# Optimization experiments

Hardware: AMD Instinct MI355X
Metric: run time of the kernel (lower is better)

The kernel has to match this reference:

```python
import jax, jax.numpy as jnp
import numpy as np

B, H, W, C = 16, 64, 64, 192
NH, WS, SHIFT = 6, 8, 4          # heads, window size, shift (window//2)
DEPTH, MLP_R = 2, 4
N = WS * WS                      # tokens per window = 64
HD = C // NH                     # head dim = 32
SCALE = HD ** -0.5
TBL = (2 * WS - 1) ** 2          # relative-bias table size = 225
NW = (H // WS) * (W // WS)       # windows per image = 64


def _rel_pos_index():
    coords = np.stack(np.meshgrid(np.arange(WS), np.arange(WS), indexing='ij')).reshape(2, -1)
    rel = (coords[:, :, None] - coords[:, None, :]).transpose(1, 2, 0)
    rel[..., 0] += WS - 1
    rel[..., 1] += WS - 1
    rel[..., 0] *= 2 * WS - 1
    return jnp.asarray(rel.sum(-1))  # [N, N] int


def _attn_mask():
    # Swin shifted-window mask: region ids then pairwise -100 where ids differ.
    img = np.zeros((H, W))
    sl = (slice(0, -WS), slice(-WS, -SHIFT), slice(-SHIFT, None))
    cnt = 0
    for hs in sl:
        for ws in sl:
            img[hs, ws] = cnt
            cnt += 1
    mw = img.reshape(H // WS, WS, W // WS, WS).transpose(0, 2, 1, 3).reshape(-1, N)
    diff = mw[:, None, :] - mw[:, :, None]
    return jnp.asarray(np.where(diff != 0, -100.0, 0.0).astype(np.float32))  # [NW, N, N]


REL_IDX = _rel_pos_index()
ATTN_MASK = _attn_mask()


def _ln(x, g, b, eps=1e-5):
    mu = x.mean(-1, keepdims=True)
    var = ((x - mu) ** 2).mean(-1, keepdims=True)
    return (x - mu) * jax.lax.rsqrt(var + eps) * g + b


def setup_inputs() -> dict:
    key = jax.random.key(0)
    ks = jax.random.split(key, 8)
    s = 0.02
    return {
        'x': jax.random.normal(ks[0], (B, H * W, C), jnp.float32),
        'norm1_g': jnp.ones((DEPTH, C)), 'norm1_b': jnp.zeros((DEPTH, C)),
        'qkv_w': jax.random.normal(ks[1], (DEPTH, 3 * C, C)) * s,
        'qkv_b': jnp.zeros((DEPTH, 3 * C)),
        'bias_table': jax.random.normal(ks[2], (DEPTH, TBL, NH)) * s,
        'proj_w': jax.random.normal(ks[3], (DEPTH, C, C)) * s,
        'proj_b': jnp.zeros((DEPTH, C)),
        'norm2_g': jnp.ones((DEPTH, C)), 'norm2_b': jnp.zeros((DEPTH, C)),
        'fc1_w': jax.random.normal(ks[4], (DEPTH, MLP_R * C, C)) * s,
        'fc1_b': jnp.zeros((DEPTH, MLP_R * C)),
        'fc2_w': jax.random.normal(ks[5], (DEPTH, C, MLP_R * C)) * s,
        'fc2_b': jnp.zeros((DEPTH, C)),
    }


def _block(x, shift, n1g, n1b, qw, qb, tbl, pw, pb, n2g, n2b, f1w, f1b, f2w, f2b):
    shortcut = x
    y = _ln(x, n1g, n1b).reshape(B, H, W, C)
    if shift > 0:
        y = jnp.roll(y, (-shift, -shift), axis=(1, 2))
    # window partition -> [B*NW, N, C]
    win = y.reshape(B, H // WS, WS, W // WS, WS, C).transpose(0, 1, 3, 2, 4, 5).reshape(-1, N, C)
    qkv = (win @ qw.T + qb).reshape(-1, N, 3, NH, HD).transpose(2, 0, 3, 1, 4)
    q, k, v = qkv[0] * SCALE, qkv[1], qkv[2]          # each [B*NW, NH, N, HD]
    attn = jnp.einsum('bhnd,bhmd->bhnm', q, k)
    attn = attn + tbl[REL_IDX].transpose(2, 0, 1)[None]  # relative position bias
    if shift > 0:
        attn = (attn.reshape(B, NW, NH, N, N) + ATTN_MASK[None, :, None]).reshape(-1, NH, N, N)
    attn = jax.nn.softmax(attn, axis=-1)
    o = jnp.einsum('bhnm,bhmd->bhnd', attn, v).transpose(0, 2, 1, 3).reshape(-1, N, C)
    o = o @ pw.T + pb
    # window reverse
    y = o.reshape(B, H // WS, W // WS, WS, WS, C).transpose(0, 1, 3, 2, 4, 5).reshape(B, H, W, C)
    if shift > 0:
        y = jnp.roll(y, (shift, shift), axis=(1, 2))
    x = shortcut + y.reshape(B, H * W, C)
    h = _ln(x, n2g, n2b)
    h = jax.nn.gelu(h @ f1w.T + f1b, approximate=False)  # torch nn.GELU = exact erf
    return x + (h @ f2w.T + f2b)


def reference(x, norm1_g, norm1_b, qkv_w, qkv_b, bias_table, proj_w, proj_b,
              norm2_g, norm2_b, fc1_w, fc1_b, fc2_w, fc2_b):
    for i in range(DEPTH):
        shift = 0 if i % 2 == 0 else SHIFT
        x = _block(x, shift, norm1_g[i], norm1_b[i], qkv_w[i], qkv_b[i], bias_table[i],
                   proj_w[i], proj_b[i], norm2_g[i], norm2_b[i],
                   fc1_w[i], fc1_b[i], fc2_w[i], fc2_b[i])
    return x
```

## Files before the change

kernel.cpp:

```cpp
#include <hip/hip_runtime.h>
#include <hip/hip_bf16.h>
#include <math.h>

typedef __hip_bfloat16 bf16;
typedef short bf16x8 __attribute__((ext_vector_type(8)));
typedef short s16x4 __attribute__((ext_vector_type(4)));
typedef float f32x4 __attribute__((ext_vector_type(4)));

#define TOKENS 65536
#define C_ 192

__device__ __forceinline__ float b2f(bf16 v){ return __bfloat162float(v); }
__device__ __forceinline__ bf16 f2b(float v){ return __float2bfloat16(v); }
__device__ __forceinline__ short f2s(float v){
  bf16 b = __float2bfloat16(v);
  union { bf16 b; short s; } u; u.b = b; return u.s;
}
__device__ __forceinline__ float s2f(short s){
  union { unsigned u; float f; } c; c.u = ((unsigned)(unsigned short)s) << 16; return c.f;
}

struct WPtrs { const void* p[13]; };
#define W_TOTAL_ 892480
#define NELEM_ (TOKENS*C_)
__global__ void convert_k(WPtrs wp, const void* __restrict__ x,
                          bf16* __restrict__ canon, float* __restrict__ xf){
  const int offs[13] = {0, 384, 768, 221952, 223104, 225856, 299584,
                        299968, 300352, 300736, 595648, 597184, 892096};
  const int lens[13] = {384, 384, 221184, 1152, 2700, 73728, 384,
                        384, 384, 294912, 1536, 294912, 384};
  int flag = (*(const unsigned*)wp.p[0] == 0x3F800000u) ? 1 : 0;
  int i = blockIdx.x*blockDim.x + threadIdx.x;
  if (i < W_TOTAL_){
    int t = 0;
    while (t < 12 && i >= offs[t+1]) t++;
    int j = i - offs[t];
    if (j < lens[t]){
      if (flag) canon[i] = f2b(((const float*)wp.p[t])[j]);
      else      canon[i] = ((const bf16*)wp.p[t])[j];
    }
  } else {
    int j = i - W_TOTAL_;
    if (j < NELEM_){
      if (flag) xf[j] = ((const float*)x)[j];
      else      xf[j] = b2f(((const bf16*)x)[j]);
    }
  }
}
__global__ void outconv_k(const float* __restrict__ x, void* __restrict__ y, int n,
                          const unsigned* __restrict__ g){
  int flag = (g[0] == 0x3F800000u) ? 1 : 0;
  int i = blockIdx.x*blockDim.x + threadIdx.x;
  if (i >= n) return;
  if (flag) ((float*)y)[i] = x[i];
  else      ((bf16*)y)[i]  = f2b(x[i]);
}

__global__ void setup_k(const bf16* __restrict__ bt, float* __restrict__ biasF,
                        const bf16* __restrict__ f1w, const bf16* __restrict__ f2w,
                        bf16* __restrict__ w1p, bf16* __restrict__ w2p){
  int idx = blockIdx.x*blockDim.x + threadIdx.x;
  if (idx < 2*6*64*64){
    int v = idx & 63;
    int lane = (idx >> 6) & 63;
    int rest = idx >> 12;
    int head = rest % 6, dd = rest / 6;
    int jt = v >> 4, it = (v >> 2) & 3, r = v & 3;
    int quad = lane >> 4, lr = lane & 15;
    int j = jt*16 + quad*4 + r;
    int i = it*16 + lr;
    int rel = ((i>>3) - (j>>3) + 7)*15 + ((i&7) - (j&7) + 7);
    biasF[idx] = b2f(bt[(dd*225 + rel)*6 + head]);
    return;
  }
  int id = idx - 2*6*64*64;
  if (id >= 589824) return;
  int arr = id / 294912;
  int r = id % 294912;
  int d = r / 147456;
  int e = r % 147456;
  int j = e & 7, lane = (e >> 3) & 63, frag = e >> 9;
  int lr = lane & 15, quad = lane >> 4;
  if (arr == 0){
    int ks = frag % 6, t = frag / 6;
    int mh = t & 1, cc = t >> 1;
    w1p[(size_t)d*147456 + e] =
        f1w[(size_t)d*147456 + (size_t)(cc*32 + mh*16 + lr)*192 + ks*32 + quad*8 + j];
  } else {
    int ct = frag % 12, cc = frag / 12;
    w2p[(size_t)d*147456 + e] =
        f2w[(size_t)d*147456 + (size_t)(ct*16 + lr)*768 + cc*32 + quad*8 + j];
  }
}

__global__ __launch_bounds__(768, 1) void attn_fused_k(float* __restrict__ xres,
    const bf16* __restrict__ n1g, const bf16* __restrict__ n1b,
    const bf16* __restrict__ qw, const bf16* __restrict__ qb,
    const bf16* __restrict__ pw, const bf16* __restrict__ pb,
    const float* __restrict__ biasF, int shift)
{
  extern __shared__ char smem[];
  short* xo = (short*)smem;
  int win = blockIdx.x;
  int tid = threadIdx.x;
  int wave = tid >> 6, lane = tid & 63;
  int quad = lane >> 4, lr = lane & 15;
  int head = wave >> 1, half = wave & 1;
  int b_ = win >> 6, wl = win & 63, wh = wl >> 3, wwi = wl & 7;
  short* kh  = (short*)(smem + 25600 + head*18432);
  short* vth = kh + 2560;
  short* qP  = vth + 2304;

  int c0 = lane*3;
  float g0 = b2f(n1g[c0]), g1 = b2f(n1g[c0+1]), g2 = b2f(n1g[c0+2]);
  float e0 = b2f(n1b[c0]), e1 = b2f(n1b[c0+1]), e2 = b2f(n1b[c0+2]);
  #pragma unroll
  for (int p = 0; p < 6; p++){
    int tok = p*12 + wave;
    if (tok < 64){
      int hh = (wh*8 + (tok>>3) + shift) & 63, ww = (wwi*8 + (tok&7) + shift) & 63;
      const float* rowp = xres + ((size_t)(b_<<12) + (hh<<6) + ww)*C_;
      float v0 = rowp[c0], v1 = rowp[c0+1], v2 = rowp[c0+2];
      float s = v0+v1+v2;
      #pragma unroll
      for (int off=32; off; off>>=1) s += __shfl_xor(s, off);
      float mu = s * (1.0f/192.0f);
      float d0=v0-mu, d1=v1-mu, d2=v2-mu;
      float q = d0*d0+d1*d1+d2*d2;
      #pragma unroll
      for (int off=32; off; off>>=1) q += __shfl_xor(q, off);
      float rstd = rsqrtf(q*(1.0f/192.0f) + 1e-5f);
      xo[tok*200 + c0]   = f2s(d0*rstd*g0 + e0);
      xo[tok*200 + c0+1] = f2s(d1*rstd*g1 + e1);
      xo[tok*200 + c0+2] = f2s(d2*rstd*g2 + e2);
    }
  }
  __syncthreads();

  const short* qwd = (const short*)qw;
  #pragma unroll
  for (int cc = 0; cc < 3; cc++){
    int nbase = cc*192 + head*32;
    f32x4 acc[2][2];
    #pragma unroll
    for (int mt = 0; mt < 2; mt++)
      #pragma unroll
      for (int nt = 0; nt < 2; nt++) acc[mt][nt] = (f32x4){0.f,0.f,0.f,0.f};
    #pragma unroll
    for (int ks = 0; ks < 6; ks++){
      bf16x8 af[2], bx[2];
      #pragma unroll
      for (int mt = 0; mt < 2; mt++)
        af[mt] = *(const bf16x8*)(qwd + (size_t)(nbase + mt*16 + lr)*192 + ks*32 + quad*8);
      #pragma unroll
      for (int nt = 0; nt < 2; nt++)
        bx[nt] = *(const bf16x8*)&xo[((2*half + nt)*16 + lr)*200 + ks*32 + quad*8];
      #pragma unroll
      for (int mt = 0; mt < 2; mt++)
        #pragma unroll
        for (int nt = 0; nt < 2; nt++)
          acc[mt][nt] = __builtin_amdgcn_mfma_f32_16x16x32_bf16(af[mt], bx[nt], acc[mt][nt], 0, 0, 0);
    }
    #pragma unroll
    for (int mt = 0; mt < 2; mt++){
      float bv[4];
      #pragma unroll
      for (int r = 0; r < 4; r++) bv[r] = b2f(qb[nbase + mt*16 + quad*4 + r]);
      #pragma unroll
      for (int nt = 0; nt < 2; nt++){
        int tok = (2*half + nt)*16 + lr;
        if (cc == 0){
          s16x4 pk;
          #pragma unroll
          for (int r = 0; r < 4; r++) pk[r] = f2s((acc[mt][nt][r] + bv[r]) * 0.17677669529663689f);
          *(s16x4*)&qP[tok*40 + mt*16 + quad*4] = pk;
        } else if (cc == 1){
          s16x4 pk;
          #pragma unroll
          for (int r = 0; r < 4; r++) pk[r] = f2s(acc[mt][nt][r] + bv[r]);
          *(s16x4*)&kh[tok*40 + mt*16 + quad*4] = pk;
        } else {
          #pragma unroll
          for (int r = 0; r < 4; r++)
            vth[(mt*16 + quad*4 + r)*72 + tok] = f2s(acc[mt][nt][r] + bv[r]);
        }
      }
    }
  }
  __syncthreads();

  bf16x8 ak[4], bq[2];
  #pragma unroll
  for (int jt = 0; jt < 4; jt++) ak[jt] = *(const bf16x8*)&kh[(jt*16 + lr)*40 + quad*8];
  #pragma unroll
  for (int it = 0; it < 2; it++)
    bq[it] = *(const bf16x8*)&qP[((2*half + it)*16 + lr)*40 + quad*8];
  __syncthreads();

  f32x4 S[4][2];
  #pragma unroll
  for (int jt = 0; jt < 4; jt++)
    #pragma unroll
    for (int it = 0; it < 2; it++) S[jt][it] = (f32x4){0.f,0.f,0.f,0.f};
  #pragma unroll
  for (int jt = 0; jt < 4; jt++)
    #pragma unroll
    for (int it = 0; it < 2; it++)
      S[jt][it] = __builtin_amdgcn_mfma_f32_16x16x32_bf16(ak[jt], bq[it], S[jt][it], 0, 0, 0);

  const f32x4* bm = (const f32x4*)(biasF + ((size_t)head*64 + lane)*64);
  #pragma unroll
  for (int jt = 0; jt < 4; jt++)
    #pragma unroll
    for (int it = 0; it < 2; it++) S[jt][it] += bm[jt*4 + 2*half + it];

  if (shift){
    int idi[2];
    #pragma unroll
    for (int it = 0; it < 2; it++){
      int itg = 2*half + it;
      int hh = wh*8 + itg*2 + (lr >> 3);
      int wwc = wwi*8 + (lr & 7);
      idi[it] = (hh < 56 ? 0 : (hh < 60 ? 1 : 2))*3 + (wwc < 56 ? 0 : (wwc < 60 ? 1 : 2));
    }
    #pragma unroll
    for (int jt = 0; jt < 4; jt++)
      #pragma unroll
      for (int r = 0; r < 4; r++){
        int j = jt*16 + quad*4 + r;
        int hh = wh*8 + (j >> 3), wwc = wwi*8 + (j & 7);
        int idj = (hh < 56 ? 0 : (hh < 60 ? 1 : 2))*3 + (wwc < 56 ? 0 : (wwc < 60 ? 1 : 2));
        #pragma unroll
        for (int it = 0; it < 2; it++)
          if (idj != idi[it]) S[jt][it][r] -= 100.f;
      }
  }
  #pragma unroll
  for (int it = 0; it < 2; it++){
    float m = -1e30f;
    #pragma unroll
    for (int jt = 0; jt < 4; jt++)
      #pragma unroll
      for (int r = 0; r < 4; r++) m = fmaxf(m, S[jt][it][r]);
    m = fmaxf(m, __shfl_xor(m, 16));
    m = fmaxf(m, __shfl_xor(m, 32));
    float s = 0.f;
    #pragma unroll
    for (int jt = 0; jt < 4; jt++)
      #pragma unroll
      for (int r = 0; r < 4; r++){
        float e = __expf(S[jt][it][r] - m);
        S[jt][it][r] = e; s += e;
      }
    s += __shfl_xor(s, 16);
    s += __shfl_xor(s, 32);
    float inv = 1.0f / s;
    #pragma unroll
    for (int jt = 0; jt < 4; jt++){
      s16x4 pk;
      #pragma unroll
      for (int r = 0; r < 4; r++) pk[r] = f2s(S[jt][it][r] * inv);
      *(s16x4*)&qP[((2*half + it)*16 + lr)*68 + jt*16 + quad*4] = pk;
    }
  }
  __syncthreads();

  bf16x8 va[2][2], pv[2][2];
  #pragma unroll
  for (int mt = 0; mt < 2; mt++)
    #pragma unroll
    for (int ks = 0; ks < 2; ks++)
      va[mt][ks] = *(const bf16x8*)&vth[(mt*16 + lr)*72 + ks*32 + quad*8];
  #pragma unroll
  for (int nt = 0; nt < 2; nt++)
    #pragma unroll
    for (int ks = 0; ks < 2; ks++)
      pv[nt][ks] = *(const bf16x8*)&qP[((2*half + nt)*16 + lr)*68 + ks*32 + quad*8];

  f32x4 O[2][2];
  #pragma unroll
  for (int mt = 0; mt < 2; mt++)
    #pragma unroll
    for (int nt = 0; nt < 2; nt++) O[mt][nt] = (f32x4){0.f,0.f,0.f,0.f};
  #pragma unroll
  for (int mt = 0; mt < 2; mt++)
    #pragma unroll
    for (int nt = 0; nt < 2; nt++)
      #pragma unroll
      for (int ks = 0; ks < 2; ks++)
        O[mt][nt] = __builtin_amdgcn_mfma_f32_16x16x32_bf16(va[mt][ks], pv[nt][ks], O[mt][nt], 0, 0, 0);

  #pragma unroll
  for (int mt = 0; mt < 2; mt++)
    #pragma unroll
    for (int nt = 0; nt < 2; nt++){
      s16x4 pk;
      #pragma unroll
      for (int r = 0; r < 4; r++) pk[r] = f2s(O[mt][nt][r]);
      *(s16x4*)&xo[((2*half + nt)*16 + lr)*200 + head*32 + mt*16 + quad*4] = pk;
    }
  __syncthreads();

  int wm = wave / 6, wn = wave % 6;
  f32x4 po[2][2];
  #pragma unroll
  for (int mt = 0; mt < 2; mt++)
    #pragma unroll
    for (int nt = 0; nt < 2; nt++) po[mt][nt] = (f32x4){0.f,0.f,0.f,0.f};
  const short* pwd = (const short*)pw;
  #pragma unroll
  for (int ks = 0; ks < 6; ks++){
    bf16x8 ao[2], bw[2];
    #pragma unroll
    for (int mt = 0; mt < 2; mt++)
      ao[mt] = *(const bf16x8*)&xo[(wm*32 + mt*16 + lr)*200 + ks*32 + quad*8];
    #pragma unroll
    for (int nt = 0; nt < 2; nt++)
      bw[nt] = *(const bf16x8*)(pwd + (size_t)(wn*32 + nt*16 + lr)*192 + ks*32 + quad*8);
    #pragma unroll
    for (int mt = 0; mt < 2; mt++)
      #pragma unroll
      for (int nt = 0; nt < 2; nt++)
        po[mt][nt] = __builtin_amdgcn_mfma_f32_16x16x32_bf16(ao[mt], bw[nt], po[mt][nt], 0, 0, 0);
  }
  #pragma unroll
  for (int nt = 0; nt < 2; nt++){
    int n = wn*32 + nt*16 + lr;
    float bv = b2f(pb[n]);
    #pragma unroll
    for (int mt = 0; mt < 2; mt++){
      #pragma unroll
      for (int r = 0; r < 4; r++){
        int tok = wm*32 + mt*16 + quad*4 + r;
        int hh = (wh*8 + (tok>>3) + shift) & 63, ww = (wwi*8 + (tok&7) + shift) & 63;
        float* dst = xres + ((size_t)(b_<<12) + (hh<<6) + ww)*C_ + n;
        *dst += po[mt][nt][r] + bv;
      }
    }
  }
}

__global__ __launch_bounds__(256, 2) void mlp_coop32_k(float* __restrict__ xres,
    const bf16* __restrict__ n2g, const bf16* __restrict__ n2b,
    const bf16* __restrict__ w1p, const bf16* __restrict__ f1b,
    const bf16* __restrict__ w2p, const bf16* __restrict__ f2bv)
{
  __shared__ short Wst[2][24*512];
  __shared__ short HsAll[4][32*36];
  int tid = threadIdx.x;
  int wave = tid >> 6, lane = tid & 63;
  int quad = lane >> 4, lr = lane & 15;
  short* Hs = HsAll[wave];
  int t0 = blockIdx.x*128 + wave*32;

  const short* w1 = (const short*)w1p;
  const short* w2 = (const short*)w2p;

  int f0 = wave*6;

  bf16x8 rg[6];
  #pragma unroll
  for (int k = 0; k < 6; k++){
    int f = f0 + k;
    const short* g = (f < 12) ? (w1 + (size_t)f*512 + lane*8)
                              : (w2 + (size_t)(f - 12)*512 + lane*8);
    rg[k] = *(const bf16x8*)g;
  }

  bf16x8 xh[2][6];
  #pragma unroll
  for (int nt = 0; nt < 2; nt++){
    const float* rowp = xres + (size_t)(t0 + nt*16 + lr)*C_;
    float v[6][8];
    float s = 0.f;
    #pragma unroll
    for (int ks = 0; ks < 6; ks++){
      int cb = ks*32 + quad*8;
      #pragma unroll
      for (int j = 0; j < 8; j++){ v[ks][j] = rowp[cb+j]; s += v[ks][j]; }
    }
    s += __shfl_xor(s, 16); s += __shfl_xor(s, 32);
    float mu = s*(1.0f/192.0f);
    float q = 0.f;
    #pragma unroll
    for (int ks = 0; ks < 6; ks++)
      #pragma unroll
      for (int j = 0; j < 8; j++){ float d = v[ks][j]-mu; q += d*d; }
    q += __shfl_xor(q, 16); q += __shfl_xor(q, 32);
    float rstd = rsqrtf(q*(1.0f/192.0f) + 1e-5f);
    #pragma unroll
    for (int ks = 0; ks < 6; ks++){
      int cb = ks*32 + quad*8;
      #pragma unroll
      for (int j = 0; j < 8; j++)
        xh[nt][ks][j] = f2s((v[ks][j]-mu)*rstd*b2f(n2g[cb+j]) + b2f(n2b[cb+j]));
    }
  }

  #pragma unroll
  for (int k = 0; k < 6; k++)
    *(bf16x8*)&Wst[0][(f0 + k)*512 + lane*8] = rg[k];

  f32x4 acc[12][2];
  #pragma unroll
  for (int ct = 0; ct < 12; ct++)
    #pragma unroll
    for (int nt = 0; nt < 2; nt++) acc[ct][nt] = (f32x4){0.f,0.f,0.f,0.f};

  int cur = 0;
  for (int cc = 0; cc < 24; cc++){
    if (cc < 23){
      #pragma unroll
      for (int k = 0; k < 6; k++){
        int f = f0 + k;
        const short* g = (f < 12) ? (w1 + (size_t)((cc+1)*12 + f)*512 + lane*8)
                                  : (w2 + (size_t)((cc+1)*12 + (f - 12))*512 + lane*8);
        rg[k] = *(const bf16x8*)g;
      }
    }

    __syncthreads();

    const short* rdb = &Wst[cur][0];

    f32x4 hacc[2][2];
    #pragma unroll
    for (int mh = 0; mh < 2; mh++)
      #pragma unroll
      for (int nt = 0; nt < 2; nt++) hacc[mh][nt] = (f32x4){0.f,0.f,0.f,0.f};
    #pragma unroll
    for (int ks = 0; ks < 6; ks++){
      bf16x8 af0 = *(const bf16x8*)&rdb[ks*512 + lane*8];
      bf16x8 af1 = *(const bf16x8*)&rdb[(6 + ks)*512 + lane*8];
      hacc[0][0] = __builtin_amdgcn_mfma_f32_16x16x32_bf16(af0, xh[0][ks], hacc[0][0], 0, 0, 0);
      hacc[0][1] = __builtin_amdgcn_mfma_f32_16x16x32_bf16(af0, xh[1][ks], hacc[0][1], 0, 0, 0);
      hacc[1][0] = __builtin_amdgcn_mfma_f32_16x16x32_bf16(af1, xh[0][ks], hacc[1][0], 0, 0, 0);
      hacc[1][1] = __builtin_amdgcn_mfma_f32_16x16x32_bf16(af1, xh[1][ks], hacc[1][1], 0, 0, 0);
    }
    #pragma unroll
    for (int mh = 0; mh < 2; mh++){
      s16x4 bb = *(const s16x4*)((const short*)f1b + cc*32 + mh*16 + quad*4);
      #pragma unroll
      for (int nt = 0; nt < 2; nt++){
        s16x4 pk;
        #pragma unroll
        for (int r = 0; r < 4; r++){
          float x = hacc[mh][nt][r] + s2f(bb[r]);
          float y = x*(0.7978845608f + 0.0356774081f*x*x);
          float t = __expf(2.0f*fminf(y, 9.0f));
          pk[r] = f2s(x*t/(t + 1.0f));
        }
        *(s16x4*)&Hs[(nt*16 + lr)*36 + mh*16 + quad*4] = pk;
      }
    }
    bf16x8 ah0 = *(const bf16x8*)&Hs[lr*36 + quad*8];
    bf16x8 ah1 = *(const bf16x8*)&Hs[(16 + lr)*36 + quad*8];
    #pragma unroll
    for (int ct = 0; ct < 12; ct++){
      bf16x8 bw = *(const bf16x8*)&rdb[(12 + ct)*512 + lane*8];
      acc[ct][0] = __builtin_amdgcn_mfma_f32_16x16x32_bf16(bw, ah0, acc[ct][0], 0, 0, 0);
      acc[ct][1] = __builtin_amdgcn_mfma_f32_16x16x32_bf16(bw, ah1, acc[ct][1], 0, 0, 0);
    }

    if (cc < 23){
      #pragma unroll
      for (int k = 0; k < 6; k++)
        *(bf16x8*)&Wst[cur ^ 1][(f0 + k)*512 + lane*8] = rg[k];
    }
    cur ^= 1;
  }

  #pragma unroll
  for (int nt = 0; nt < 2; nt++){
    int m = t0 + nt*16 + lr;
    float* rowd = xres + (size_t)m*C_;
    #pragma unroll
    for (int ct = 0; ct < 12; ct++){
      int n0 = ct*16 + quad*4;
      s16x4 bb = *(const s16x4*)((const short*)f2bv + n0);
      f32x4* dst = (f32x4*)(rowd + n0);
      f32x4 cur4 = *dst;
      #pragma unroll
      for (int r = 0; r < 4; r++) cur4[r] += acc[ct][nt][r] + s2f(bb[r]);
      *dst = cur4;
    }
  }
}

extern "C" void kernel_launch(void* const* d_in, const int* in_sizes, int n_in,
                              void* d_out, int out_size, void* d_ws, size_t ws_size,
                              hipStream_t stream)
{
  (void)in_sizes; (void)n_in; (void)out_size;

  if (ws_size < (size_t)52117000) return;
  char* ws = (char*)d_ws;
  float* xf   = (float*)ws;
  bf16* canon = (bf16*)(ws + 50331648);
  float* biasF = (float*)d_out;
  bf16* w1p = (bf16*)((char*)d_out + 196608);
  bf16* w2p = (bf16*)((char*)d_out + 786432);

  static const int W_OFF[13] = {0, 384, 768, 221952, 223104, 225856, 299584,
                                299968, 300352, 300736, 595648, 597184, 892096};

  hipFuncSetAttribute((const void*)attn_fused_k,
                      hipFuncAttributeMaxDynamicSharedMemorySize, 136192);

  WPtrs wp;
  for (int i = 0; i < 13; i++) wp.p[i] = d_in[i+1];

  const int nelem = TOKENS*C_;
  convert_k<<<(W_TOTAL_ + nelem + 255)/256, 256, 0, stream>>>(wp, d_in[0], canon, xf);

  const bf16* n1g = canon + W_OFF[0];
  const bf16* n1b = canon + W_OFF[1];
  const bf16* qw  = canon + W_OFF[2];
  const bf16* qb  = canon + W_OFF[3];
  const bf16* bt  = canon + W_OFF[4];
  const bf16* pw  = canon + W_OFF[5];
  const bf16* pb  = canon + W_OFF[6];
  const bf16* n2g = canon + W_OFF[7];
  const bf16* n2b = canon + W_OFF[8];
  const bf16* f1w = canon + W_OFF[9];
  const bf16* f1b = canon + W_OFF[10];
  const bf16* f2w = canon + W_OFF[11];
  const bf16* f2bv= canon + W_OFF[12];

  setup_k<<<(49152 + 589824 + 255)/256, 256, 0, stream>>>(bt, biasF, f1w, f2w, w1p, w2p);

  for (int d = 0; d < 2; d++){
    int shift = d ? 4 : 0;
    attn_fused_k<<<1024, 768, 136192, stream>>>(xf,
        n1g + d*192, n1b + d*192, qw + d*576*192, qb + d*576,
        pw + d*192*192, pb + d*192, biasF + d*6*64*64, shift);
    mlp_coop32_k<<<512, 256, 0, stream>>>(xf,
        n2g + d*192, n2b + d*192, w1p + d*147456, f1b + d*768,
        w2p + d*147456, f2bv + d*192);
  }
  outconv_k<<<nelem/256, 256, 0, stream>>>(xf, d_out, nelem, (const unsigned*)d_in[1]);
}
```

Measured before the change: 561.9 us.

## Fuse input conversion into first attention and output conversion into last MLP

The first attention kernel now reads the raw input tensor directly (f32 or bf16) and writes the residual sum into the f32 workspace. This skips the separate full-tensor conversion pass. The final MLP kernel writes the output in its target dtype directly, removing the outconv pass. Scratch buffers move from the output into the workspace, and the fused path is enabled only when the workspace is large enough; otherwise it falls back to the old path.

```diff
diff --git a/kernel.cpp b/kernel.cpp
--- a/kernel.cpp
+++ b/kernel.cpp
@@ -97,7 +97,8 @@
     const bf16* __restrict__ n1g, const bf16* __restrict__ n1b,
     const bf16* __restrict__ qw, const bf16* __restrict__ qb,
     const bf16* __restrict__ pw, const bf16* __restrict__ pb,
-    const float* __restrict__ biasF, int shift)
+    const float* __restrict__ biasF, int shift,
+    const void* __restrict__ xraw, const unsigned* __restrict__ flagw)
 {
   extern __shared__ char smem[];
   short* xo = (short*)smem;
@@ -111,6 +112,8 @@
   short* vth = kh + 2560;
   short* qP  = vth + 2304;
 
+  int isf32 = xraw ? ((*flagw == 0x3F800000u) ? 1 : 0) : 0;
+
   int c0 = lane*3;
   float g0 = b2f(n1g[c0]), g1 = b2f(n1g[c0+1]), g2 = b2f(n1g[c0+2]);
   float e0 = b2f(n1b[c0]), e1 = b2f(n1b[c0+1]), e2 = b2f(n1b[c0+2]);
@@ -119,8 +122,20 @@
     int tok = p*12 + wave;
     if (tok < 64){
       int hh = (wh*8 + (tok>>3) + shift) & 63, ww = (wwi*8 + (tok&7) + shift) & 63;
-      const float* rowp = xres + ((size_t)(b_<<12) + (hh<<6) + ww)*C_;
-      float v0 = rowp[c0], v1 = rowp[c0+1], v2 = rowp[c0+2];
+      size_t roff = ((size_t)(b_<<12) + (hh<<6) + ww)*C_;
+      float v0, v1, v2;
+      if (xraw){
+        if (isf32){
+          const float* rowp = (const float*)xraw + roff;
+          v0 = rowp[c0]; v1 = rowp[c0+1]; v2 = rowp[c0+2];
+        } else {
+          const short* rowp = (const short*)xraw + roff;
+          v0 = s2f(rowp[c0]); v1 = s2f(rowp[c0+1]); v2 = s2f(rowp[c0+2]);
+        }
+      } else {
+        const float* rowp = xres + roff;
+        v0 = rowp[c0]; v1 = rowp[c0+1]; v2 = rowp[c0+2];
+      }
       float s = v0+v1+v2;
       #pragma unroll
       for (int off=32; off; off>>=1) s += __shfl_xor(s, off);
@@ -333,8 +348,13 @@
       for (int r = 0; r < 4; r++){
         int tok = wm*32 + mt*16 + quad*4 + r;
         int hh = (wh*8 + (tok>>3) + shift) & 63, ww = (wwi*8 + (tok&7) + shift) & 63;
-        float* dst = xres + ((size_t)(b_<<12) + (hh<<6) + ww)*C_ + n;
-        *dst += po[mt][nt][r] + bv;
+        size_t off = ((size_t)(b_<<12) + (hh<<6) + ww)*C_ + n;
+        if (xraw){
+          float base = isf32 ? ((const float*)xraw)[off] : s2f(((const short*)xraw)[off]);
+          xres[off] = base + po[mt][nt][r] + bv;
+        } else {
+          xres[off] += po[mt][nt][r] + bv;
+        }
       }
     }
   }
@@ -343,7 +363,8 @@
 __global__ __launch_bounds__(256, 2) void mlp_coop32_k(float* __restrict__ xres,
     const bf16* __restrict__ n2g, const bf16* __restrict__ n2b,
     const bf16* __restrict__ w1p, const bf16* __restrict__ f1b,
-    const bf16* __restrict__ w2p, const bf16* __restrict__ f2bv)
+    const bf16* __restrict__ w2p, const bf16* __restrict__ f2bv,
+    void* __restrict__ yout, const unsigned* __restrict__ flagw)
 {
   __shared__ short Wst[2][24*512];
   __shared__ short HsAll[4][32*36];
@@ -470,6 +491,7 @@
     cur ^= 1;
   }
 
+  int isf32 = yout ? ((*flagw == 0x3F800000u) ? 1 : 0) : 0;
   #pragma unroll
   for (int nt = 0; nt < 2; nt++){
     int m = t0 + nt*16 + lr;
@@ -483,6 +505,17 @@
       #pragma unroll
       for (int r = 0; r < 4; r++) cur4[r] += acc[ct][nt][r] + s2f(bb[r]);
       *dst = cur4;
+      if (yout){
+        size_t off = (size_t)m*C_ + n0;
+        if (isf32){
+          *(f32x4*)((float*)yout + off) = cur4;
+        } else {
+          s16x4 ob;
+          #pragma unroll
+          for (int r = 0; r < 4; r++) ob[r] = f2s(cur4[r]);
+          *(s16x4*)((short*)yout + off) = ob;
+        }
+      }
     }
   }
 }
@@ -497,9 +530,21 @@
   char* ws = (char*)d_ws;
   float* xf   = (float*)ws;
   bf16* canon = (bf16*)(ws + 50331648);
-  float* biasF = (float*)d_out;
-  bf16* w1p = (bf16*)((char*)d_out + 196608);
-  bf16* w2p = (bf16*)((char*)d_out + 786432);
+
+  const size_t SCR_OFF = 52117504;
+  bool fused = (ws_size >= SCR_OFF + 196608 + 589824 + 589824);
+
+  float* biasF;
+  bf16 *w1p, *w2p;
+  if (fused){
+    biasF = (float*)(ws + SCR_OFF);
+    w1p   = (bf16*)(ws + SCR_OFF + 196608);
+    w2p   = (bf16*)(ws + SCR_OFF + 196608 + 589824);
+  } else {
+    biasF = (float*)d_out;
+    w1p   = (bf16*)((char*)d_out + 196608);
+    w2p   = (bf16*)((char*)d_out + 786432);
+  }
 
   static const int W_OFF[13] = {0, 384, 768, 221952, 223104, 225856, 299584,
                                 299968, 300352, 300736, 595648, 597184, 892096};
@@ -511,7 +556,8 @@
   for (int i = 0; i < 13; i++) wp.p[i] = d_in[i+1];
 
   const int nelem = TOKENS*C_;
-  convert_k<<<(W_TOTAL_ + nelem + 255)/256, 256, 0, stream>>>(wp, d_in[0], canon, xf);
+  int conv_total = fused ? W_TOTAL_ : (W_TOTAL_ + nelem);
+  convert_k<<<(conv_total + 255)/256, 256, 0, stream>>>(wp, d_in[0], canon, xf);
 
   const bf16* n1g = canon + W_OFF[0];
   const bf16* n1b = canon + W_OFF[1];
@@ -529,14 +575,19 @@
 
   setup_k<<<(49152 + 589824 + 255)/256, 256, 0, stream>>>(bt, biasF, f1w, f2w, w1p, w2p);
 
+  const unsigned* flagw = (const unsigned*)d_in[1];
   for (int d = 0; d < 2; d++){
     int shift = d ? 4 : 0;
+    const void* xraw = (fused && d == 0) ? d_in[0] : nullptr;
     attn_fused_k<<<1024, 768, 136192, stream>>>(xf,
         n1g + d*192, n1b + d*192, qw + d*576*192, qb + d*576,
-        pw + d*192*192, pb + d*192, biasF + d*6*64*64, shift);
+        pw + d*192*192, pb + d*192, biasF + d*6*64*64, shift,
+        xraw, flagw);
+    void* yout = (fused && d == 1) ? d_out : nullptr;
     mlp_coop32_k<<<512, 256, 0, stream>>>(xf,
         n2g + d*192, n2b + d*192, w1p + d*147456, f1b + d*768,
-        w2p + d*147456, f2bv + d*192);
-  }
-  outconv_k<<<nelem/256, 256, 0, stream>>>(xf, d_out, nelem, (const unsigned*)d_in[1]);
-}
+        w2p + d*147456, f2bv + d*192, yout, flagw);
+  }
+  if (!fused)
+    outconv_k<<<nelem/256, 256, 0, stream>>>(xf, d_out, nelem, (const unsigned*)d_in[1]);
+}
```

Measured after the change: 546.7 us. -2.7%, faster.
